# Kernel tuning notes

Measured on AMD Instinct MI355X. Metric: run time of the kernel, lower is better.

Reference implementation:

```python
import jax, jax.numpy as jnp
import numpy as np

N_EMBD = 1024
NUM_EXPERTS = 8
TOP_K = 2
HIDDEN = 2048  # n_embd * hidden_mult(2)
AUX_COEF = 0.01
B, S = 4, 2048


def setup_inputs() -> dict:
    key = jax.random.key(0)
    k_x, k_g, k_w1, k_w2 = jax.random.split(key, 4)
    x = jax.random.normal(k_x, (B, S, N_EMBD), dtype=jnp.float32)
    # router gate: Linear(n_embd, num_experts, bias=False) -> weight (E, D), applied as x @ W^T
    gate_w = jax.random.uniform(k_g, (NUM_EXPERTS, N_EMBD), dtype=jnp.float32,
                                minval=-1.0 / np.sqrt(N_EMBD), maxval=1.0 / np.sqrt(N_EMBD))
    w1 = jax.random.uniform(k_w1, (NUM_EXPERTS, N_EMBD, HIDDEN), dtype=jnp.float32,
                            minval=-1.0 / np.sqrt(N_EMBD), maxval=1.0 / np.sqrt(N_EMBD))
    w2 = jax.random.uniform(k_w2, (NUM_EXPERTS, HIDDEN, N_EMBD), dtype=jnp.float32,
                            minval=-1.0 / np.sqrt(HIDDEN), maxval=1.0 / np.sqrt(HIDDEN))
    return {"x": x, "gate_w": gate_w, "w1": w1, "w2": w2}


def reference(x, gate_w, w1, w2):
    batch, seq, d = x.shape
    # router (token-level, no noise / eval path)
    router_logits = jnp.einsum('bsd,ed->bse', x, gate_w)          # (B,S,E)
    router_probs = jax.nn.softmax(router_logits, axis=-1)
    top_k_probs, top_k_indices = jax.lax.top_k(router_probs, TOP_K)  # (B,S,K)
    top_k_probs = top_k_probs / jnp.sum(top_k_probs, axis=-1, keepdims=True)

    # dense all-expert FFN (matches torch einsum pattern)
    x_flat = x.reshape(-1, d)                                      # (N,D), N=B*S
    hidden = jnp.einsum('nd,edh->neh', x_flat, w1)                 # (N,E,H)
    hidden = jax.nn.relu(hidden)
    expert_out = jnp.einsum('neh,ehd->ned', hidden, w2)            # (N,E,D)
    expert_out = expert_out.reshape(batch, seq, NUM_EXPERTS, d)    # (B,S,E,D)

    # gather selected experts and combine
    idx = top_k_indices[..., None]                                 # (B,S,K,1)
    selected = jnp.take_along_axis(expert_out, idx, axis=2)        # (B,S,K,D)
    output = jnp.sum(selected * top_k_probs[..., None], axis=2)    # (B,S,D)

    # load-balancing aux loss (Switch style)
    probs_flat = router_probs.reshape(-1, NUM_EXPERTS)             # (N,E)
    top_expert = jnp.argmax(probs_flat, axis=-1)                   # (N,)
    f = jnp.mean(jax.nn.one_hot(top_expert, NUM_EXPERTS, dtype=probs_flat.dtype), axis=0)
    P = jnp.mean(probs_flat, axis=0)
    aux_loss = AUX_COEF * NUM_EXPERTS * jnp.sum(f * P)
    return output, aux_loss
```

## Files before the change

### kernel.cpp

```cpp
#include <hip/hip_runtime.h>
#include <hip/hip_bf16.h>
#include <stdint.h>

#define N_TOK 8192
#define DIM   1024
#define HID   2048
#define NEXP  8
#define RB    256

typedef __bf16 bf16x8 __attribute__((ext_vector_type(8)));
typedef float  f32x4  __attribute__((ext_vector_type(4)));
typedef unsigned short u16x8 __attribute__((ext_vector_type(8)));
typedef unsigned short u16x4 __attribute__((ext_vector_type(4)));

__device__ __forceinline__ float bits2f(unsigned short u) {
    union { unsigned int i; float f; } c; c.i = ((unsigned int)u) << 16; return c.f;
}
__device__ __forceinline__ unsigned short f2bfbits(float f) {
    __hip_bfloat16 h = __float2bfloat16(f);
    return *(unsigned short*)&h;
}

__device__ __forceinline__ void load_lds16(const void* g, void* l) {
    __builtin_amdgcn_global_load_lds(
        (const __attribute__((address_space(1))) void*)g,
        (__attribute__((address_space(3))) void*)l,
        16, 0, 0);
}

__global__ __launch_bounds__(512) void route_k(
    const float* __restrict__ x,
    const float* __restrict__ gate,
    int* __restrict__ epack, float* __restrict__ pw,
    unsigned short* __restrict__ xb,
    int* __restrict__ H0, int* __restrict__ H1, float* __restrict__ Pblk)
{
    __shared__ float gwS[NEXP][16][64];
    __shared__ int h0S[NEXP], h1S[NEXP];
    __shared__ float pS[NEXP];
    int tid = threadIdx.x;
    if (tid < NEXP) { h0S[tid] = 0; h1S[tid] = 0; pS[tid] = 0.f; }
    for (int idx = tid; idx < NEXP * DIM; idx += 512) {
        int e = idx >> 10, rem = idx & 1023, i = rem >> 6, l = rem & 63;
        gwS[e][i][l] = gate[e * DIM + l * 16 + i];
    }
    __syncthreads();
    int w = tid >> 6, lane = tid & 63;
    float prAcc[NEXP];
    #pragma unroll
    for (int e = 0; e < NEXP; ++e) prAcc[e] = 0.f;
    for (int it = 0; it < 4; ++it) {
        int token = blockIdx.x * 32 + w * 4 + it;
        const float* xr = x + (size_t)token * DIM + lane * 16;
        float xv[16];
        #pragma unroll
        for (int q = 0; q < 4; ++q) {
            float4 v = *(const float4*)(xr + q * 4);
            xv[q * 4 + 0] = v.x; xv[q * 4 + 1] = v.y; xv[q * 4 + 2] = v.z; xv[q * 4 + 3] = v.w;
        }
        {
            u16x8 o0, o1;
            #pragma unroll
            for (int i = 0; i < 8; ++i) { o0[i] = f2bfbits(xv[i]); o1[i] = f2bfbits(xv[8 + i]); }
            unsigned short* dst = xb + (size_t)token * DIM + lane * 16;
            *(u16x8*)dst = o0;
            *(u16x8*)(dst + 8) = o1;
        }
        float lg[NEXP];
        #pragma unroll
        for (int e = 0; e < NEXP; ++e) {
            float s = 0.f;
            #pragma unroll
            for (int i = 0; i < 16; ++i) s += xv[i] * gwS[e][i][lane];
            lg[e] = s;
        }
        #pragma unroll
        for (int off = 32; off > 0; off >>= 1)
            #pragma unroll
            for (int e = 0; e < NEXP; ++e) lg[e] += __shfl_xor(lg[e], off);
        float mx = lg[0]; int am = 0;
        #pragma unroll
        for (int e = 1; e < NEXP; ++e) if (lg[e] > mx) { mx = lg[e]; am = e; }
        float pr[NEXP], se = 0.f;
        #pragma unroll
        for (int e = 0; e < NEXP; ++e) { pr[e] = __expf(lg[e] - mx); se += pr[e]; }
        float inv = 1.f / se;
        #pragma unroll
        for (int e = 0; e < NEXP; ++e) pr[e] *= inv;
        float m2 = -1.f; int a2 = 0;
        #pragma unroll
        for (int e = 0; e < NEXP; ++e) if (e != am && pr[e] > m2) { m2 = pr[e]; a2 = e; }
        float psum = pr[am] + m2;
        if (lane == 0) {
            epack[token] = am | (a2 << 4);
            pw[token * 2] = pr[am] / psum;
            pw[token * 2 + 1] = m2 / psum;
            atomicAdd(&h0S[am], 1);
            atomicAdd(&h1S[a2], 1);
            #pragma unroll
            for (int e = 0; e < NEXP; ++e) prAcc[e] += pr[e];
        }
    }
    if (lane == 0) {
        #pragma unroll
        for (int e = 0; e < NEXP; ++e) atomicAdd(&pS[e], prAcc[e]);
    }
    __syncthreads();
    if (tid < NEXP) {
        H0[blockIdx.x * NEXP + tid] = h0S[tid];
        H1[blockIdx.x * NEXP + tid] = h1S[tid];
        Pblk[blockIdx.x * NEXP + tid] = pS[tid];
    }
}

__global__ __launch_bounds__(256) void scan_k(
    const int* __restrict__ H0, const int* __restrict__ H1,
    const float* __restrict__ Pblk,
    int* __restrict__ bbL, int* __restrict__ counts, int* __restrict__ basep,
    float* __restrict__ aux)
{
    __shared__ int h0S[RB * NEXP], h1S[RB * NEXP], bbS[RB * NEXP];
    __shared__ float pSh[RB * NEXP];
    __shared__ int cS[NEXP], fS[NEXP];
    __shared__ float psS[NEXP];
    int tid = threadIdx.x;
    for (int i = tid; i < RB * NEXP; i += 256) { h0S[i] = H0[i]; h1S[i] = H1[i]; pSh[i] = Pblk[i]; }
    __syncthreads();
    if (tid < NEXP) {
        int run = 0, f = 0; float p = 0.f;
        for (int b = 0; b < RB; ++b) {
            int i = b * NEXP + tid;
            bbS[i] = run;
            run += h0S[i] + h1S[i];
            f += h0S[i];
            p += pSh[i];
        }
        cS[tid] = run; fS[tid] = f; psS[tid] = p;
        counts[tid] = run;
    }
    __syncthreads();
    if (tid == 0) {
        int b = 0; float s = 0.f;
        for (int e = 0; e < NEXP; ++e) {
            basep[e] = b; b += cS[e];
            s += (fS[e] * (1.f / 8192.f)) * (psS[e] * (1.f / 8192.f));
        }
        aux[0] = 0.01f * 8.f * s;
    }
    __syncthreads();
    for (int i = tid; i < RB * NEXP; i += 256) bbL[i] = bbS[i];
}

__global__ __launch_bounds__(256) void scatter_k(
    const int* __restrict__ epack, const int* __restrict__ bbL,
    int* __restrict__ tok_list, int* __restrict__ code)
{
    int tid = threadIdx.x;
    int w = tid >> 6, lane = tid & 63;
    int g = blockIdx.x * 4 + w;
    int token = g * 32 + (lane >> 1);
    int ep = epack[token];
    int e = (lane & 1) ? ((ep >> 4) & 0xF) : (ep & 0xF);
    unsigned long long lower = (lane == 0) ? 0ull : ((~0ull) >> (64 - lane));
    unsigned long long mymask = 0;
    #pragma unroll
    for (int ee = 0; ee < NEXP; ++ee) {
        unsigned long long m = __ballot(e == ee);
        if (ee == e) mymask = m;
    }
    int rank = __popcll(mymask & lower);
    int slot = bbL[g * NEXP + e] + rank;
    tok_list[e * N_TOK + slot] = token;
    code[token * 2 + (lane & 1)] = (e << 13) | slot;
}

__global__ __launch_bounds__(256) void transpose_cvt_k(const float* __restrict__ in,
                                                       unsigned short* __restrict__ out,
                                                       int R, int C)
{
    __shared__ unsigned short tile[64][72];
    int e = blockIdx.z;
    const float* inp = in + (size_t)e * R * C;
    unsigned short* outp = out + (size_t)e * R * C;
    int r0 = blockIdx.y * 64, c0 = blockIdx.x * 64;
    int tid = threadIdx.x;
    {
        int r = tid >> 2;
        int cseg = (tid & 3) * 16;
        const float* src = inp + (size_t)(r0 + r) * C + c0 + cseg;
        #pragma unroll
        for (int q = 0; q < 4; ++q) {
            float4 v = *(const float4*)(src + q * 4);
            tile[r][cseg + q * 4 + 0] = f2bfbits(v.x);
            tile[r][cseg + q * 4 + 1] = f2bfbits(v.y);
            tile[r][cseg + q * 4 + 2] = f2bfbits(v.z);
            tile[r][cseg + q * 4 + 3] = f2bfbits(v.w);
        }
    }
    __syncthreads();
    {
        int c = tid >> 2;
        int rseg = (tid & 3) * 16;
        unsigned short* dst = outp + (size_t)(c0 + c) * R + r0 + rseg;
        #pragma unroll
        for (int h = 0; h < 2; ++h) {
            u16x8 o;
            #pragma unroll
            for (int i = 0; i < 8; ++i) o[i] = tile[rseg + h * 8 + i][c];
            *(u16x8*)(dst + h * 8) = o;
        }
    }
}

template<bool GATHER, bool RELU>
__global__ __launch_bounds__(256) void moe_gemm(
    const unsigned short* __restrict__ A,
    const unsigned short* __restrict__ B,
    unsigned short* __restrict__ O,
    const int* __restrict__ counts,
    const int* __restrict__ basep,
    const int* __restrict__ tok_list,
    const int K, const int N)
{
    const int e = blockIdx.z;
    const int cnt = counts[e];
    const int m0 = blockIdx.y * 128;
    if (m0 >= cnt) return;
    const int n0 = blockIdx.x * 128;
    const int bas = basep[e];

    const int tid = threadIdx.x;
    const int w = tid >> 6, lane = tid & 63;
    const int wr = w >> 1, wc = w & 1;

    __shared__ __align__(16) unsigned short lds[8192];

    const int kc = (tid & 3) * 8;
    const int r0i = tid >> 2, r1i = 64 + (tid >> 2);
    const unsigned short *aRow0, *aRow1;
    if (GATHER) {
        int s0 = m0 + r0i, s1 = m0 + r1i;
        int t0 = (s0 < cnt) ? tok_list[e * N_TOK + s0] : 0;
        int t1 = (s1 < cnt) ? tok_list[e * N_TOK + s1] : 0;
        aRow0 = A + (size_t)t0 * K + kc;
        aRow1 = A + (size_t)t1 * K + kc;
    } else {
        int s0 = m0 + r0i; if (s0 > cnt - 1) s0 = cnt - 1;
        int s1 = m0 + r1i; if (s1 > cnt - 1) s1 = cnt - 1;
        aRow0 = A + (size_t)(bas + s0) * K + kc;
        aRow1 = A + (size_t)(bas + s1) * K + kc;
    }
    const unsigned short* Be = B + (size_t)e * N * K;
    const unsigned short* bRow0 = Be + (size_t)(n0 + r0i) * K + kc;
    const unsigned short* bRow1 = Be + (size_t)(n0 + r1i) * K + kc;

    f32x4 acc[4][4];
    #pragma unroll
    for (int i = 0; i < 4; ++i)
        #pragma unroll
        for (int j = 0; j < 4; ++j) acc[i][j] = f32x4{0.f, 0.f, 0.f, 0.f};

    const int quad = lane >> 4, ml = lane & 15;
    unsigned short* ldsA0 = &lds[tid * 8];
    unsigned short* ldsA1 = &lds[2048 + tid * 8];
    unsigned short* ldsB0 = &lds[4096 + tid * 8];
    unsigned short* ldsB1 = &lds[6144 + tid * 8];

    const int steps = K >> 5;
    for (int kt = 0; kt < steps; ++kt) {
        const int ko = kt * 32;
        load_lds16(aRow0 + ko, ldsA0);
        load_lds16(aRow1 + ko, ldsA1);
        load_lds16(bRow0 + ko, ldsB0);
        load_lds16(bRow1 + ko, ldsB1);
        __syncthreads();
        bf16x8 af[4], bfr[4];
        #pragma unroll
        for (int i = 0; i < 4; ++i)
            af[i] = *(const bf16x8*)&lds[(wr * 64 + i * 16 + ml) * 32 + quad * 8];
        #pragma unroll
        for (int j = 0; j < 4; ++j)
            bfr[j] = *(const bf16x8*)&lds[4096 + (wc * 64 + j * 16 + ml) * 32 + quad * 8];
        #pragma unroll
        for (int i = 0; i < 4; ++i)
            #pragma unroll
            for (int j = 0; j < 4; ++j)
                acc[i][j] = __builtin_amdgcn_mfma_f32_16x16x32_bf16(af[i], bfr[j], acc[i][j], 0, 0, 0);
        __syncthreads();
    }

    #pragma unroll
    for (int i = 0; i < 4; ++i) {
        int rbase = wr * 64 + i * 16 + quad * 4;
        #pragma unroll
        for (int r = 0; r < 4; ++r) {
            int slot = m0 + rbase + r;
            if (slot < cnt) {
                unsigned short* orow = O + (size_t)(bas + slot) * N + n0 + wc * 64 + ml;
                #pragma unroll
                for (int j = 0; j < 4; ++j) {
                    float v = acc[i][j][r];
                    if (RELU) v = v > 0.f ? v : 0.f;
                    orow[j * 16] = f2bfbits(v);
                }
            }
        }
    }
}

__global__ __launch_bounds__(256) void combine_k(
    const unsigned short* __restrict__ Yp,
    const int* __restrict__ code, const float* __restrict__ pw,
    const int* __restrict__ basep,
    float* __restrict__ out)
{
    int t = blockIdx.x;
    int c0 = code[t * 2], c1 = code[t * 2 + 1];
    float p0 = pw[t * 2], p1 = pw[t * 2 + 1];
    size_t r0 = (size_t)(basep[c0 >> 13] + (c0 & 0x1FFF)) * DIM;
    size_t r1 = (size_t)(basep[c1 >> 13] + (c1 & 0x1FFF)) * DIM;
    int d = threadIdx.x * 4;
    u16x4 a = *(const u16x4*)(Yp + r0 + d);
    u16x4 b = *(const u16x4*)(Yp + r1 + d);
    float4 o;
    o.x = p0 * bits2f(a[0]) + p1 * bits2f(b[0]);
    o.y = p0 * bits2f(a[1]) + p1 * bits2f(b[1]);
    o.z = p0 * bits2f(a[2]) + p1 * bits2f(b[2]);
    o.w = p0 * bits2f(a[3]) + p1 * bits2f(b[3]);
    *(float4*)(out + (size_t)t * DIM + d) = o;
}

extern "C" void kernel_launch(void* const* d_in, const int* in_sizes, int n_in,
                              void* d_out, int out_size, void* d_ws, size_t ws_size,
                              hipStream_t stream)
{
    const float* x    = (const float*)d_in[0];
    const float* gate = (const float*)d_in[1];
    const float* w1   = (const float*)d_in[2];
    const float* w2   = (const float*)d_in[3];
    float* out = (float*)d_out;

    char* ws = (char*)d_ws;
    int*   counts   = (int*)(ws + 0);
    int*   basep    = (int*)(ws + 256);
    int*   epack    = (int*)(ws + 1024);
    int*   H0       = (int*)(ws + 1024 + 32768);
    int*   H1       = (int*)(ws + 1024 + 40960);
    float* Pblk     = (float*)(ws + 1024 + 49152);
    int*   bbL      = (int*)(ws + 1024 + 57344);
    int*   tok_list = (int*)(ws + 131072);
    int*   code     = (int*)(ws + 131072 + 262144);
    float* pw       = (float*)(ws + 131072 + 262144 + 65536);
    unsigned short* w1t    = (unsigned short*)(ws + (1 << 20));
    unsigned short* w2t    = (unsigned short*)(ws + (1 << 20) + 33554432);
    unsigned short* hidden = (unsigned short*)(ws + (1 << 20) + 67108864);
    unsigned short* YpXb   = (unsigned short*)(ws + (1 << 20) + 67108864 + 67108864);
    unsigned short* xb     = YpXb;
    unsigned short* Yp     = YpXb;

    route_k<<<RB, 512, 0, stream>>>(x, gate, epack, pw, xb, H0, H1, Pblk);
    scan_k<<<1, 256, 0, stream>>>(H0, H1, Pblk, bbL, counts, basep, out + (size_t)N_TOK * DIM);
    scatter_k<<<64, 256, 0, stream>>>(epack, bbL, tok_list, code);
    transpose_cvt_k<<<dim3(HID / 64, DIM / 64, NEXP), 256, 0, stream>>>(w1, w1t, DIM, HID);
    transpose_cvt_k<<<dim3(DIM / 64, HID / 64, NEXP), 256, 0, stream>>>(w2, w2t, HID, DIM);
    moe_gemm<true, true><<<dim3(HID / 128, 64, NEXP), 256, 0, stream>>>(
        xb, w1t, hidden, counts, basep, tok_list, DIM, HID);
    moe_gemm<false, false><<<dim3(DIM / 128, 64, NEXP), 256, 0, stream>>>(
        hidden, w2t, Yp, counts, basep, tok_list, HID, DIM);
    combine_k<<<N_TOK, 256, 0, stream>>>(Yp, code, pw, basep, out);
}
```

Measured before the change: 446.7 us.

## Split-K the second expert GEMM and XOR-swizzle LDS tiles

Splits the second MoE GEMM (K=2048) into two K-halves, each written to its own bf16 partial buffer, and has the combine kernel sum the two partials. This doubles the grid for the down-projection to improve occupancy and load balance. It also XOR-swizzles the LDS layout of the A/B tiles to reduce bank conflicts on fragment reads. In exchange it adds extra partial-output traffic, rounds each partial to bf16 before summing, and reuses the w1t buffer as scratch for the second partial.

```diff
diff --git a/kernel.cpp b/kernel.cpp
--- a/kernel.cpp
+++ b/kernel.cpp
@@ -212,17 +212,28 @@
     }
 }
 
-template<bool GATHER, bool RELU>
+template<bool GATHER, bool RELU, bool SPLITK>
 __global__ __launch_bounds__(256) void moe_gemm(
     const unsigned short* __restrict__ A,
     const unsigned short* __restrict__ B,
-    unsigned short* __restrict__ O,
+    unsigned short* __restrict__ O0,
+    unsigned short* __restrict__ O1,
     const int* __restrict__ counts,
     const int* __restrict__ basep,
     const int* __restrict__ tok_list,
     const int K, const int N)
 {
-    const int e = blockIdx.z;
+    int e, koff, steps;
+    unsigned short* O;
+    if (SPLITK) {
+        e = blockIdx.z >> 1;
+        int kp = blockIdx.z & 1;
+        koff = kp * (K >> 1);
+        steps = K >> 6;
+        O = kp ? O1 : O0;
+    } else {
+        e = blockIdx.z; koff = 0; steps = K >> 5; O = O0;
+    }
     const int cnt = counts[e];
     const int m0 = blockIdx.y * 128;
     if (m0 >= cnt) return;
@@ -235,24 +246,24 @@
 
     __shared__ __align__(16) unsigned short lds[8192];
 
-    const int kc = (tid & 3) * 8;
+    const int kc = ((tid & 3) ^ ((tid >> 3) & 3)) * 8;
     const int r0i = tid >> 2, r1i = 64 + (tid >> 2);
     const unsigned short *aRow0, *aRow1;
     if (GATHER) {
         int s0 = m0 + r0i, s1 = m0 + r1i;
         int t0 = (s0 < cnt) ? tok_list[e * N_TOK + s0] : 0;
         int t1 = (s1 < cnt) ? tok_list[e * N_TOK + s1] : 0;
-        aRow0 = A + (size_t)t0 * K + kc;
-        aRow1 = A + (size_t)t1 * K + kc;
+        aRow0 = A + (size_t)t0 * K + koff + kc;
+        aRow1 = A + (size_t)t1 * K + koff + kc;
     } else {
         int s0 = m0 + r0i; if (s0 > cnt - 1) s0 = cnt - 1;
         int s1 = m0 + r1i; if (s1 > cnt - 1) s1 = cnt - 1;
-        aRow0 = A + (size_t)(bas + s0) * K + kc;
-        aRow1 = A + (size_t)(bas + s1) * K + kc;
+        aRow0 = A + (size_t)(bas + s0) * K + koff + kc;
+        aRow1 = A + (size_t)(bas + s1) * K + koff + kc;
     }
     const unsigned short* Be = B + (size_t)e * N * K;
-    const unsigned short* bRow0 = Be + (size_t)(n0 + r0i) * K + kc;
-    const unsigned short* bRow1 = Be + (size_t)(n0 + r1i) * K + kc;
+    const unsigned short* bRow0 = Be + (size_t)(n0 + r0i) * K + koff + kc;
+    const unsigned short* bRow1 = Be + (size_t)(n0 + r1i) * K + koff + kc;
 
     f32x4 acc[4][4];
     #pragma unroll
@@ -266,7 +277,15 @@
     unsigned short* ldsB0 = &lds[4096 + tid * 8];
     unsigned short* ldsB1 = &lds[6144 + tid * 8];
 
-    const int steps = K >> 5;
+    int offA[4], offB[4];
+    #pragma unroll
+    for (int i = 0; i < 4; ++i) {
+        int Ra = wr * 64 + i * 16 + ml;
+        offA[i] = Ra * 32 + ((quad ^ ((Ra >> 1) & 3)) * 8);
+        int Rb = wc * 64 + i * 16 + ml;
+        offB[i] = 4096 + Rb * 32 + ((quad ^ ((Rb >> 1) & 3)) * 8);
+    }
+
     for (int kt = 0; kt < steps; ++kt) {
         const int ko = kt * 32;
         load_lds16(aRow0 + ko, ldsA0);
@@ -276,11 +295,9 @@
         __syncthreads();
         bf16x8 af[4], bfr[4];
         #pragma unroll
-        for (int i = 0; i < 4; ++i)
-            af[i] = *(const bf16x8*)&lds[(wr * 64 + i * 16 + ml) * 32 + quad * 8];
-        #pragma unroll
-        for (int j = 0; j < 4; ++j)
-            bfr[j] = *(const bf16x8*)&lds[4096 + (wc * 64 + j * 16 + ml) * 32 + quad * 8];
+        for (int i = 0; i < 4; ++i) af[i] = *(const bf16x8*)&lds[offA[i]];
+        #pragma unroll
+        for (int j = 0; j < 4; ++j) bfr[j] = *(const bf16x8*)&lds[offB[j]];
         #pragma unroll
         for (int i = 0; i < 4; ++i)
             #pragma unroll
@@ -309,7 +326,8 @@
 }
 
 __global__ __launch_bounds__(256) void combine_k(
-    const unsigned short* __restrict__ Yp,
+    const unsigned short* __restrict__ Y0,
+    const unsigned short* __restrict__ Y1,
     const int* __restrict__ code, const float* __restrict__ pw,
     const int* __restrict__ basep,
     float* __restrict__ out)
@@ -320,13 +338,15 @@
     size_t r0 = (size_t)(basep[c0 >> 13] + (c0 & 0x1FFF)) * DIM;
     size_t r1 = (size_t)(basep[c1 >> 13] + (c1 & 0x1FFF)) * DIM;
     int d = threadIdx.x * 4;
-    u16x4 a = *(const u16x4*)(Yp + r0 + d);
-    u16x4 b = *(const u16x4*)(Yp + r1 + d);
+    u16x4 a0 = *(const u16x4*)(Y0 + r0 + d);
+    u16x4 a1 = *(const u16x4*)(Y1 + r0 + d);
+    u16x4 b0 = *(const u16x4*)(Y0 + r1 + d);
+    u16x4 b1 = *(const u16x4*)(Y1 + r1 + d);
     float4 o;
-    o.x = p0 * bits2f(a[0]) + p1 * bits2f(b[0]);
-    o.y = p0 * bits2f(a[1]) + p1 * bits2f(b[1]);
-    o.z = p0 * bits2f(a[2]) + p1 * bits2f(b[2]);
-    o.w = p0 * bits2f(a[3]) + p1 * bits2f(b[3]);
+    o.x = p0 * (bits2f(a0[0]) + bits2f(a1[0])) + p1 * (bits2f(b0[0]) + bits2f(b1[0]));
+    o.y = p0 * (bits2f(a0[1]) + bits2f(a1[1])) + p1 * (bits2f(b0[1]) + bits2f(b1[1]));
+    o.z = p0 * (bits2f(a0[2]) + bits2f(a1[2])) + p1 * (bits2f(b0[2]) + bits2f(b1[2]));
+    o.w = p0 * (bits2f(a0[3]) + bits2f(a1[3])) + p1 * (bits2f(b0[3]) + bits2f(b1[3]));
     *(float4*)(out + (size_t)t * DIM + d) = o;
 }
 
@@ -354,18 +374,18 @@
     unsigned short* w1t    = (unsigned short*)(ws + (1 << 20));
     unsigned short* w2t    = (unsigned short*)(ws + (1 << 20) + 33554432);
     unsigned short* hidden = (unsigned short*)(ws + (1 << 20) + 67108864);
-    unsigned short* YpXb   = (unsigned short*)(ws + (1 << 20) + 67108864 + 67108864);
-    unsigned short* xb     = YpXb;
-    unsigned short* Yp     = YpXb;
+    unsigned short* xb     = (unsigned short*)(ws + (1 << 20) + 134217728);
+    unsigned short* Yp0    = xb;
+    unsigned short* Yp1    = w1t;
 
     route_k<<<RB, 512, 0, stream>>>(x, gate, epack, pw, xb, H0, H1, Pblk);
     scan_k<<<1, 256, 0, stream>>>(H0, H1, Pblk, bbL, counts, basep, out + (size_t)N_TOK * DIM);
     scatter_k<<<64, 256, 0, stream>>>(epack, bbL, tok_list, code);
     transpose_cvt_k<<<dim3(HID / 64, DIM / 64, NEXP), 256, 0, stream>>>(w1, w1t, DIM, HID);
     transpose_cvt_k<<<dim3(DIM / 64, HID / 64, NEXP), 256, 0, stream>>>(w2, w2t, HID, DIM);
-    moe_gemm<true, true><<<dim3(HID / 128, 64, NEXP), 256, 0, stream>>>(
-        xb, w1t, hidden, counts, basep, tok_list, DIM, HID);
-    moe_gemm<false, false><<<dim3(DIM / 128, 64, NEXP), 256, 0, stream>>>(
-        hidden, w2t, Yp, counts, basep, tok_list, HID, DIM);
-    combine_k<<<N_TOK, 256, 0, stream>>>(Yp, code, pw, basep, out);
-}
+    moe_gemm<true, true, false><<<dim3(HID / 128, 64, NEXP), 256, 0, stream>>>(
+        xb, w1t, hidden, nullptr, counts, basep, tok_list, DIM, HID);
+    moe_gemm<false, false, true><<<dim3(DIM / 128, 64, NEXP * 2), 256, 0, stream>>>(
+        hidden, w2t, Yp0, Yp1, counts, basep, tok_list, HID, DIM);
+    combine_k<<<N_TOK, 256, 0, stream>>>(Yp0, Yp1, code, pw, basep, out);
+}
```

New measurement: 428.4 us. -4.1%, faster.
